# Optimization experiments

Hardware: AMD Instinct MI355X
Metric: run time of the kernel (lower is better)

## Reference

```python
import jax, jax.numpy as jnp
import numpy as np

B, S, H, V = 32, 400, 512, 50000


def setup_inputs() -> dict:
    key = jax.random.key(0)
    ks = jax.random.split(key, 32)
    g = lambda i, shape: jax.random.normal(ks[i], shape, jnp.float32) * 0.05
    return {
        "x_id": jax.random.randint(ks[0], (B, S), 0, V, jnp.int32),
        "y_id": jax.random.randint(ks[1], (B, 1), 0, V, jnp.int32),
        "x_mask": jnp.zeros((B, S), jnp.int32),  # pad flag: 1 = pad
        "emb": g(2, (V, H)),
        "enc_fw_W": g(3, (H, 3 * H)), "enc_fw_U": g(4, (H, 3 * H)), "enc_fw_b": g(5, (2, 3 * H)),
        "enc_bw_W": g(6, (H, 3 * H)), "enc_bw_U": g(7, (H, 3 * H)), "enc_bw_b": g(8, (2, 3 * H)),
        "red_W": g(9, (2 * H, H)), "red_b": g(10, (H,)),
        "dec_W": g(11, (H, 3 * H)), "dec_U": g(12, (H, 3 * H)), "dec_b": g(13, (2, 3 * H)),
        "att_Wh": g(14, (2 * H, H)), "att_Ws": g(15, (H, H)), "att_bs": g(16, (H,)),
        "att_Wc": g(17, (1, 1)), "att_V": g(18, (H, 1)),
        "fc_W": g(19, (3 * H, H)), "fc_b": g(20, (H,)),
        "vocab_W": g(21, (H, V)),
        "pg_Wh": g(22, (2 * H, 1)), "pg_Ws": g(23, (H, 1)), "pg_Wx": g(24, (H, 1)), "pg_b": g(25, (1,)),
    }


def _gru_cell(h, xz, U, br):
    # Keras GRU, reset_after=True, gate order z, r, h
    hd = h.shape[-1]
    rec = h @ U + br
    z = jax.nn.sigmoid(xz[..., :hd] + rec[..., :hd])
    r = jax.nn.sigmoid(xz[..., hd:2 * hd] + rec[..., hd:2 * hd])
    hh = jnp.tanh(xz[..., 2 * hd:] + r * rec[..., 2 * hd:])
    return z * h + (1.0 - z) * hh


def _gru_scan(x, h0, W, U, b):
    xz = x @ W + b[0]  # [b,T,3H] -- input projections precomputed
    def step(h, xt):
        h = _gru_cell(h, xt, U, b[1])
        return h, h
    h_last, hs = jax.lax.scan(step, h0, jnp.swapaxes(xz, 0, 1))
    return jnp.swapaxes(hs, 0, 1), h_last


def reference(x_id, y_id, x_mask, emb, enc_fw_W, enc_fw_U, enc_fw_b, enc_bw_W, enc_bw_U, enc_bw_b,
              red_W, red_b, dec_W, dec_U, dec_b, att_Wh, att_Ws, att_bs, att_Wc, att_V,
              fc_W, fc_b, vocab_W, pg_Wh, pg_Ws, pg_Wx, pg_b):
    b, s = x_id.shape
    hid = enc_fw_U.shape[0]
    maskf = x_mask.astype(jnp.float32)
    # ---- encoder: single-layer BiGRU ----
    x_emb = emb[x_id]                                     # [b,S,H]
    h0 = jnp.zeros((b, hid), x_emb.dtype)
    fw_seq, fw_s = _gru_scan(x_emb, h0, enc_fw_W, enc_fw_U, enc_fw_b)
    bw_seq, bw_s = _gru_scan(x_emb[:, ::-1], h0, enc_bw_W, enc_bw_U, enc_bw_b)
    enc_seq = jnp.concatenate([fw_seq, bw_seq[:, ::-1]], -1)   # [b,S,2H]
    state = jax.nn.relu(jnp.concatenate([fw_s, bw_s], -1) @ red_W + red_b)  # [b,H]
    # ---- decoder: one GRU step ----
    y_emb = emb[y_id]                                     # [b,1,H]
    xz = y_emb[:, 0] @ dec_W + dec_b[0]
    dec_state = _gru_cell(state, xz, dec_U, dec_b[1])     # [b,H]
    dec_out = dec_state[:, None, :]                       # [b,1,H]
    # ---- Bahdanau attention with (zero-initialized) coverage ----
    e = enc_seq @ att_Wh + (dec_out @ att_Ws + att_bs)    # [b,S,H]
    cover = jnp.zeros((b, s, 1), e.dtype)
    e = e + cover @ att_Wc
    e = jnp.tanh(e) @ att_V                               # [b,S,1]
    e = e + maskf[..., None] * -1e10
    w = jax.nn.softmax(e, axis=-2)                        # [b,S,1]
    context = jnp.sum(w * enc_seq, axis=-2, keepdims=True)  # [b,1,2H]
    # ---- output projection + vocab softmax ----
    y_out = jnp.concatenate([dec_out, context], -1) @ fc_W + fc_b  # [b,1,H]
    vocab_dist = jax.nn.softmax(y_out[:, 0] @ vocab_W, axis=-1)    # [b,V]
    # ---- pointer gate ----
    p_gen = jax.nn.sigmoid(context[:, 0] @ pg_Wh + dec_state @ pg_Ws + y_emb[:, 0] @ pg_Wx + pg_b)  # [b,1]
    # ---- extended-vocab copy distribution (vectorized batched scatter-add) ----
    aw = w[..., 0] * (1.0 - maskf) * (1.0 - p_gen)        # [b,S]
    ext = jnp.pad(p_gen * vocab_dist, ((0, 0), (0, s)))   # [b,V+S]
    bidx = jnp.arange(b)[:, None]
    final = ext.at[bidx, x_id].add(aw)                    # [b,V+S]
    return final
```

## Files before the change

### kernel.cpp

```cpp
#include <hip/hip_runtime.h>
#include <math.h>

#define S_LEN 400
#define BATCH 32
#define HID   512
#define G3    1536
#define N2    3072
#define VOC   50000
#define OUTW  (VOC + S_LEN)

typedef unsigned long long ull;
typedef unsigned int uint;
typedef unsigned short ushort;
typedef short bf16x8 __attribute__((ext_vector_type(8)));
typedef float f32x4 __attribute__((ext_vector_type(4)));
typedef ushort u16x8 __attribute__((ext_vector_type(8)));

__device__ __forceinline__ float sigf(float x) { return 1.f / (1.f + __expf(-x)); }
__device__ __forceinline__ float tanh_fast(float x) {
  const float xc = fminf(fmaxf(x, -15.f), 15.f);
  const float e = __expf(-2.f * xc);
  return (1.f - e) / (1.f + e);
}
__device__ __forceinline__ ushort f2bf(float f) {
  uint u = __float_as_uint(f);
  u += 0x7FFFu + ((u >> 16) & 1u);
  return (ushort)(u >> 16);
}
__device__ __forceinline__ float bf2f(ushort h) {
  return __uint_as_float((uint)h << 16);
}
__device__ __forceinline__ float dot4(float4 a, float4 b) {
  return a.x*b.x + a.y*b.y + a.z*b.z + a.w*b.w;
}

__device__ void trans_tile_512(const float* __restrict__ srcA,
                               const float* __restrict__ srcB,
                               const int split, const int stride, const int Krows,
                               const int k0, const int n0,
                               ushort* __restrict__ dstH, float* __restrict__ dstF)
{
  __shared__ float tt[64][65];
  const int tid = threadIdx.x;
  const int j = tid & 63, i0 = tid >> 6;
  {
    const int n = n0 + j;
    const float* s = (n < split) ? (srcA + n) : (srcB + (n - split));
    #pragma unroll
    for (int i = i0; i < 64; i += 8)
      tt[i][j] = s[(size_t)(k0 + i) * stride];
  }
  __syncthreads();
  const int ii = tid & 63;
  if (dstH != nullptr) {
    #pragma unroll
    for (int jj = i0; jj < 64; jj += 8)
      dstH[(size_t)(n0 + jj) * Krows + k0 + ii] = f2bf(tt[ii][jj]);
  } else {
    #pragma unroll
    for (int jj = i0; jj < 64; jj += 8)
      dstF[(size_t)(n0 + jj) * Krows + k0 + ii] = tt[ii][jj];
  }
}

__global__ __launch_bounds__(512) void gru_scan(
    const ushort* __restrict__ xzm,
    const ushort* __restrict__ Utbf,
    const float* __restrict__ bfw, const float* __restrict__ bbw,
    float* __restrict__ enc_seq, ushort* __restrict__ enc_bf,
    ull* __restrict__ hpkt,
    const float* __restrict__ att_Wh, const float* __restrict__ red_W,
    const float* __restrict__ dec_W, const float* __restrict__ dec_U,
    const float* __restrict__ att_Ws, const float* __restrict__ fc_W,
    ushort* __restrict__ Whbf, float* __restrict__ redWt,
    float* __restrict__ decWUt, float* __restrict__ WsT,
    float* __restrict__ fcT)
{
  if (blockIdx.x >= 128) {
    const int tb = blockIdx.x - 128;
    if (tb < 128) {
      trans_tile_512(att_Wh, att_Wh, 512, 512, 1024,
                     (tb % 16) * 64, (tb / 16) * 64, Whbf, nullptr);
    } else if (tb < 256) {
      const int t = tb - 128;
      trans_tile_512(red_W, red_W, 512, 512, 1024,
                     (t % 16) * 64, (t / 16) * 64, nullptr, redWt);
    } else if (tb < 640) {
      const int t = tb - 256;
      trans_tile_512(dec_W, dec_U, G3, G3, 512,
                     (t % 8) * 64, (t / 8) * 64, nullptr, decWUt);
    } else if (tb < 704) {
      const int t = tb - 640;
      trans_tile_512(att_Ws, att_Ws, 512, 512, 512,
                     (t % 8) * 64, (t / 8) * 64, nullptr, WsT);
    } else {
      const int t = tb - 704;
      trans_tile_512(fc_W, fc_W, 512, 512, 1536,
                     (t % 24) * 64, (t / 24) * 64, nullptr, fcT);
    }
    return;
  }

  const int bid = blockIdx.x;
  const int group = bid & 7;
  const int dir = group >> 2;
  const int bg  = group & 3;
  const int ht  = bid >> 3;
  const int tid = threadIdx.x;
  const int lane = tid & 63;
  const int w  = tid >> 6;
  const int l15 = lane & 15;
  const int lk  = lane >> 4;

  const float* __restrict__ br = (dir ? bbw : bfw) + G3;

  const int gate = w % 3, jh = w / 3;
  bf16x8 ufrag[16];
  if (w < 6) {
    const ushort* ub = Utbf + ((size_t)dir * G3 + gate * 512 + ht * 32 + jh * 16 + l15) * 512
                     + lk * 8;
    #pragma unroll
    for (int s = 0; s < 16; ++s)
      ufrag[s] = *(const bf16x8*)(ub + s * 32);
  }

  __shared__ ushort h_bf[16][520];
  __shared__ float redm[3][8][32];

  for (int i = tid; i < 16 * 520; i += 512) ((ushort*)h_bf)[i] = 0;

  const int cb = w;
  const int gbi = tid >> 5;
  const int gj  = tid & 31;
  const int gjq = ht * 32 + gj;
  const int gb  = bg * 8 + (gbi & 7);
  const float brz = br[gjq], brr = br[512 + gjq], brh = br[1024 + gjq];

  ull* __restrict__ pk = hpkt + (size_t)dir * (2 * BATCH * HID);
  __syncthreads();

  for (int t = 0; t < S_LEN; ++t) {
    const int ts = dir ? (S_LEN - 1 - t) : t;

    float xzv0 = 0.f, xzv1 = 0.f, xzv2 = 0.f;
    if (tid < 256) {
      const ushort* xp = xzm + ((size_t)gb * S_LEN + ts) * N2 + dir * G3 + gjq;
      xzv0 = bf2f(xp[0]); xzv1 = bf2f(xp[512]); xzv2 = bf2f(xp[1024]);
    }

    float hold = 0.f;
    {
      ull* bp = pk + ((size_t)(t & 1) * BATCH + (bg * 8 + cb)) * HID + lane;
      ull* hp = pk + ((size_t)(t & 1) * BATCH + gb) * HID + gjq;
      const uint tu = (uint)t;
      for (;;) {
        ull v0 = __hip_atomic_load(bp,       __ATOMIC_RELAXED, __HIP_MEMORY_SCOPE_AGENT);
        ull v1 = __hip_atomic_load(bp + 64,  __ATOMIC_RELAXED, __HIP_MEMORY_SCOPE_AGENT);
        ull v2 = __hip_atomic_load(bp + 128, __ATOMIC_RELAXED, __HIP_MEMORY_SCOPE_AGENT);
        ull v3 = __hip_atomic_load(bp + 192, __ATOMIC_RELAXED, __HIP_MEMORY_SCOPE_AGENT);
        ull v4 = __hip_atomic_load(bp + 256, __ATOMIC_RELAXED, __HIP_MEMORY_SCOPE_AGENT);
        ull v5 = __hip_atomic_load(bp + 320, __ATOMIC_RELAXED, __HIP_MEMORY_SCOPE_AGENT);
        ull v6 = __hip_atomic_load(bp + 384, __ATOMIC_RELAXED, __HIP_MEMORY_SCOPE_AGENT);
        ull v7 = __hip_atomic_load(bp + 448, __ATOMIC_RELAXED, __HIP_MEMORY_SCOPE_AGENT);
        bool ok = ((uint)(v0 >> 32) == tu) & ((uint)(v1 >> 32) == tu)
                & ((uint)(v2 >> 32) == tu) & ((uint)(v3 >> 32) == tu)
                & ((uint)(v4 >> 32) == tu) & ((uint)(v5 >> 32) == tu)
                & ((uint)(v6 >> 32) == tu) & ((uint)(v7 >> 32) == tu);
        ull hv = 0;
        if (tid < 256) {
          hv = __hip_atomic_load(hp, __ATOMIC_RELAXED, __HIP_MEMORY_SCOPE_AGENT);
          ok &= ((uint)(hv >> 32) == tu);
        }
        if (__all(ok)) {
          h_bf[cb][lane]       = f2bf(__uint_as_float((uint)v0));
          h_bf[cb][lane + 64]  = f2bf(__uint_as_float((uint)v1));
          h_bf[cb][lane + 128] = f2bf(__uint_as_float((uint)v2));
          h_bf[cb][lane + 192] = f2bf(__uint_as_float((uint)v3));
          h_bf[cb][lane + 256] = f2bf(__uint_as_float((uint)v4));
          h_bf[cb][lane + 320] = f2bf(__uint_as_float((uint)v5));
          h_bf[cb][lane + 384] = f2bf(__uint_as_float((uint)v6));
          h_bf[cb][lane + 448] = f2bf(__uint_as_float((uint)v7));
          if (tid < 256) hold = __uint_as_float((uint)hv);
          break;
        }
        __builtin_amdgcn_s_sleep(1);
      }
    }
    __syncthreads();

    if (w < 6) {
      f32x4 acc = f32x4{0.f, 0.f, 0.f, 0.f};
      #pragma unroll
      for (int s = 0; s < 16; ++s) {
        const bf16x8 af = *(const bf16x8*)&h_bf[l15][s * 32 + lk * 8];
        acc = __builtin_amdgcn_mfma_f32_16x16x32_bf16(af, ufrag[s], acc, 0, 0, 0);
      }
      if (lk < 2) {
        #pragma unroll
        for (int r = 0; r < 4; ++r)
          redm[gate][lk * 4 + r][jh * 16 + l15] = acc[r];
      }
    }
    __syncthreads();

    if (tid < 256) {
      const float rz = redm[0][gbi][gj] + brz;
      const float rr = redm[1][gbi][gj] + brr;
      const float rh = redm[2][gbi][gj] + brh;
      const float z  = sigf(xzv0 + rz);
      const float r  = sigf(xzv1 + rr);
      const float hh = tanh_fast(xzv2 + r * rh);
      const float hnew = z * hold + (1.f - z) * hh;
      const ull pack = ((ull)(uint)(t + 1) << 32) | (ull)__float_as_uint(hnew);
      __hip_atomic_store(pk + ((size_t)((t + 1) & 1) * BATCH + gb) * HID + gjq,
                         pack, __ATOMIC_RELAXED, __HIP_MEMORY_SCOPE_AGENT);
      const size_t eidx = ((size_t)gb * S_LEN + ts) * 1024 + dir * 512 + gjq;
      enc_seq[eidx] = hnew;
      enc_bf[eidx]  = f2bf(hnew);
    }
    __syncthreads();
  }
}

__global__ __launch_bounds__(256) void k_cvtA(
    const int* __restrict__ x_id, const float* __restrict__ emb,
    ushort* __restrict__ Abf)
{
  const int tid = threadIdx.x;
  const int row = blockIdx.x * 4 + (tid >> 6);
  const int k8 = (tid & 63) * 8;
  const int rid = x_id[row];
  const float4 e0 = *(const float4*)&emb[(size_t)rid * 512 + k8];
  const float4 e1 = *(const float4*)&emb[(size_t)rid * 512 + k8 + 4];
  u16x8 o;
  o[0] = f2bf(e0.x); o[1] = f2bf(e0.y); o[2] = f2bf(e0.z); o[3] = f2bf(e0.w);
  o[4] = f2bf(e1.x); o[5] = f2bf(e1.y); o[6] = f2bf(e1.z); o[7] = f2bf(e1.w);
  *(u16x8*)&Abf[(size_t)row * 512 + k8] = o;
}

__global__ __launch_bounds__(256) void k_transUp(
    const float* __restrict__ fwW, const float* __restrict__ bwW,
    const float* __restrict__ fwb, const float* __restrict__ bwb,
    const float* __restrict__ fwU, const float* __restrict__ bwU,
    ushort* __restrict__ Wt, float* __restrict__ bm,
    ushort* __restrict__ Utbf)
{
  __shared__ float tt[64][65];
  const int b = blockIdx.x;
  const int tid = threadIdx.x;
  const int j = tid & 63, i0 = tid >> 6;
  const float* srcA; const float* srcB; int split, k0, n0; ushort* dst;
  if (b < 384)      { srcA = fwW; srcB = bwW; split = G3;
                      k0 = (b % 8) * 64; n0 = (b / 8) * 64; dst = Wt; }
  else if (b < 576) { const int t = b - 384; srcA = fwU; srcB = fwU; split = N2;
                      k0 = (t % 8) * 64; n0 = (t / 8) * 64; dst = Utbf; }
  else              { const int t = b - 576; srcA = bwU; srcB = bwU; split = N2;
                      k0 = (t % 8) * 64; n0 = (t / 8) * 64;
                      dst = Utbf + (size_t)G3 * 512; }
  {
    const int n = n0 + j;
    const float* s = (n < split) ? (srcA + n) : (srcB + (n - split));
    #pragma unroll
    for (int i = i0; i < 64; i += 4)
      tt[i][j] = s[(size_t)(k0 + i) * G3];
  }
  __syncthreads();
  const int ii = tid & 63;
  #pragma unroll
  for (int jj = i0; jj < 64; jj += 4)
    dst[(size_t)(n0 + jj) * 512 + k0 + ii] = f2bf(tt[ii][jj]);
  if (b < 384 && k0 == 0 && tid < 64) {
    const int n = n0 + tid;
    bm[n] = (n < G3) ? fwb[n] : bwb[n - G3];
  }
}

__global__ __launch_bounds__(256) void gemm_bf16(
    const ushort* __restrict__ A,
    const ushort* __restrict__ Bt,
    const float* __restrict__ bias,
    ushort* __restrict__ C)
{
  const int m0 = blockIdx.y * 128, n0 = blockIdx.x * 128;
  const int tid = threadIdx.x;
  const int w = tid >> 6, lane = tid & 63;
  const int l15 = lane & 15, lk = lane >> 4;
  __shared__ short As[128][40];
  __shared__ short Bs[128][40];
  f32x4 acc[2][8];
  #pragma unroll
  for (int i = 0; i < 2; ++i)
    #pragma unroll
    for (int j = 0; j < 8; ++j) acc[i][j] = f32x4{0.f, 0.f, 0.f, 0.f};

  const int sr = tid >> 1;
  const int sc = (tid & 1) * 8;

  for (int k0 = 0; k0 < 512; k0 += 32) {
    const uint4 a0 = *(const uint4*)&A[(size_t)(m0 + sr) * 512 + k0 + sc];
    const uint4 a1 = *(const uint4*)&A[(size_t)(m0 + sr) * 512 + k0 + 16 + sc];
    const uint4 b0 = *(const uint4*)&Bt[(size_t)(n0 + sr) * 512 + k0 + sc];
    const uint4 b1 = *(const uint4*)&Bt[(size_t)(n0 + sr) * 512 + k0 + 16 + sc];
    *(uint4*)&As[sr][sc]      = a0;
    *(uint4*)&As[sr][16 + sc] = a1;
    *(uint4*)&Bs[sr][sc]      = b0;
    *(uint4*)&Bs[sr][16 + sc] = b1;
    __syncthreads();

    bf16x8 af[2], bfr[8];
    #pragma unroll
    for (int rf = 0; rf < 2; ++rf)
      af[rf] = *(const bf16x8*)&As[w * 32 + rf * 16 + l15][lk * 8];
    #pragma unroll
    for (int cf = 0; cf < 8; ++cf)
      bfr[cf] = *(const bf16x8*)&Bs[cf * 16 + l15][lk * 8];
    #pragma unroll
    for (int rf = 0; rf < 2; ++rf)
      #pragma unroll
      for (int cf = 0; cf < 8; ++cf)
        acc[rf][cf] = __builtin_amdgcn_mfma_f32_16x16x32_bf16(
            af[rf], bfr[cf], acc[rf][cf], 0, 0, 0);
    __syncthreads();
  }

  #pragma unroll
  for (int rf = 0; rf < 2; ++rf) {
    #pragma unroll
    for (int cf = 0; cf < 8; ++cf) {
      const int col = n0 + cf * 16 + l15;
      const float bv = bias[col];
      const int rowb = m0 + w * 32 + rf * 16 + lk * 4;
      #pragma unroll
      for (int r = 0; r < 4; ++r)
        C[(size_t)(rowb + r) * N2 + col] = f2bf(acc[rf][cf][r] + bv);
    }
  }
}

__global__ __launch_bounds__(256) void gemm_att(
    const ushort* __restrict__ A,
    const ushort* __restrict__ Bt,
    const float* __restrict__ dterm,
    const float* __restrict__ attV,
    float* __restrict__ e_part)
{
  const int m0 = blockIdx.y * 128, n0 = blockIdx.x * 128;
  const int tid = threadIdx.x;
  const int w = tid >> 6, lane = tid & 63;
  const int l15 = lane & 15, lk = lane >> 4;
  __shared__ short As[128][40];
  __shared__ short Bs[128][40];
  f32x4 acc[2][8];
  #pragma unroll
  for (int i = 0; i < 2; ++i)
    #pragma unroll
    for (int j = 0; j < 8; ++j) acc[i][j] = f32x4{0.f, 0.f, 0.f, 0.f};

  const int sr = tid >> 1;
  const int sc = (tid & 1) * 8;

  for (int k0 = 0; k0 < 1024; k0 += 32) {
    const uint4 a0 = *(const uint4*)&A[(size_t)(m0 + sr) * 1024 + k0 + sc];
    const uint4 a1 = *(const uint4*)&A[(size_t)(m0 + sr) * 1024 + k0 + 16 + sc];
    const uint4 b0 = *(const uint4*)&Bt[(size_t)(n0 + sr) * 1024 + k0 + sc];
    const uint4 b1 = *(const uint4*)&Bt[(size_t)(n0 + sr) * 1024 + k0 + 16 + sc];
    *(uint4*)&As[sr][sc]      = a0;
    *(uint4*)&As[sr][16 + sc] = a1;
    *(uint4*)&Bs[sr][sc]      = b0;
    *(uint4*)&Bs[sr][16 + sc] = b1;
    __syncthreads();

    bf16x8 af[2], bfr[8];
    #pragma unroll
    for (int rf = 0; rf < 2; ++rf)
      af[rf] = *(const bf16x8*)&As[w * 32 + rf * 16 + l15][lk * 8];
    #pragma unroll
    for (int cf = 0; cf < 8; ++cf)
      bfr[cf] = *(const bf16x8*)&Bs[cf * 16 + l15][lk * 8];
    #pragma unroll
    for (int rf = 0; rf < 2; ++rf)
      #pragma unroll
      for (int cf = 0; cf < 8; ++cf)
        acc[rf][cf] = __builtin_amdgcn_mfma_f32_16x16x32_bf16(
            af[rf], bfr[cf], acc[rf][cf], 0, 0, 0);
    __syncthreads();
  }

  #pragma unroll
  for (int rf = 0; rf < 2; ++rf) {
    #pragma unroll
    for (int r = 0; r < 4; ++r) {
      const int row = m0 + w * 32 + rf * 16 + lk * 4 + r;
      const int b = row / S_LEN;
      float p = 0.f;
      #pragma unroll
      for (int cf = 0; cf < 8; ++cf) {
        const int col = n0 + cf * 16 + l15;
        p += attV[col] * tanh_fast(acc[rf][cf][r] + dterm[(size_t)b * 512 + col]);
      }
      p += __shfl_xor(p, 1); p += __shfl_xor(p, 2);
      p += __shfl_xor(p, 4); p += __shfl_xor(p, 8);
      if (l15 == 0) e_part[(size_t)row * 4 + blockIdx.x] = p;
    }
  }
}

__global__ __launch_bounds__(128) void k_state(const float* __restrict__ enc,
    const float* __restrict__ redWt,
    const float* __restrict__ red_b, float* __restrict__ state)
{
  const int b = blockIdx.y;
  const int j = blockIdx.x*128 + threadIdx.x;
  const float4* wr = (const float4*)(redWt + (size_t)j * 1024);
  const float4* fw = (const float4*)(enc + ((size_t)b*S_LEN + (S_LEN-1))*1024);
  const float4* bw = (const float4*)(enc + ((size_t)b*S_LEN)*1024 + 512);
  float acc = red_b[j];
  #pragma unroll 4
  for (int k = 0; k < 128; ++k) acc += dot4(fw[k], wr[k]);
  #pragma unroll 4
  for (int k = 0; k < 128; ++k) acc += dot4(bw[k], wr[128 + k]);
  state[(size_t)b*512 + j] = fmaxf(acc, 0.f);
}

__global__ __launch_bounds__(128) void k_dec(
    const int* __restrict__ y_id, const float* __restrict__ emb,
    const float* __restrict__ state,
    const float* __restrict__ decWUt,
    const float* __restrict__ dec_b, float* __restrict__ dst)
{
  const int b = blockIdx.y;
  const int j = blockIdx.x*128 + threadIdx.x;
  const float4* ye = (const float4*)(emb + (size_t)y_id[b] * 512);
  const float4* st = (const float4*)(state + (size_t)b * 512);
  const float4* w0 = (const float4*)(decWUt + (size_t)(j)        * 512);
  const float4* w1 = (const float4*)(decWUt + (size_t)(512  + j) * 512);
  const float4* w2 = (const float4*)(decWUt + (size_t)(1024 + j) * 512);
  const float4* u0 = (const float4*)(decWUt + (size_t)(G3 + j)        * 512);
  const float4* u1 = (const float4*)(decWUt + (size_t)(G3 + 512  + j) * 512);
  const float4* u2 = (const float4*)(decWUt + (size_t)(G3 + 1024 + j) * 512);
  float xz0 = dec_b[j], xz1 = dec_b[512+j], xz2 = dec_b[1024+j];
  float rc0 = dec_b[G3+j], rc1 = dec_b[G3+512+j], rc2 = dec_b[G3+1024+j];
  #pragma unroll 2
  for (int k = 0; k < 128; ++k) {
    const float4 yv = ye[k], sv = st[k];
    xz0 += dot4(yv, w0[k]); xz1 += dot4(yv, w1[k]); xz2 += dot4(yv, w2[k]);
    rc0 += dot4(sv, u0[k]); rc1 += dot4(sv, u1[k]); rc2 += dot4(sv, u2[k]);
  }
  const float z  = sigf(xz0 + rc0);
  const float r  = sigf(xz1 + rc1);
  const float hh = tanh_fast(xz2 + r*rc2);
  const float sj = state[(size_t)b*512 + j];
  dst[(size_t)b*512 + j] = z*sj + (1.f-z)*hh;
}

__global__ __launch_bounds__(128) void k_dterm(const float* __restrict__ dec,
    const float* __restrict__ WsT,
    const float* __restrict__ att_bs, float* __restrict__ dterm)
{
  const int b = blockIdx.y;
  const int j = blockIdx.x*128 + threadIdx.x;
  const float4* d = (const float4*)(dec + (size_t)b*512);
  const float4* wr = (const float4*)(WsT + (size_t)j * 512);
  float acc = att_bs[j];
  #pragma unroll 4
  for (int k = 0; k < 128; ++k) acc += dot4(d[k], wr[k]);
  dterm[(size_t)b*512 + j] = acc;
}

__global__ __launch_bounds__(512) void k_soft(const float* __restrict__ e_part,
    const int* __restrict__ x_mask, float* __restrict__ wat)
{
  const int b = blockIdx.x, tid = threadIdx.x;
  __shared__ float sm[512];
  float e = -1e30f, ev = 0.f;
  if (tid < S_LEN) {
    const float* ep = e_part + (size_t)(b*S_LEN + tid)*4;
    ev = ep[0]+ep[1]+ep[2]+ep[3] + (float)x_mask[b*S_LEN+tid] * -1e10f;
    e = ev;
  }
  sm[tid] = e; __syncthreads();
  for (int s = 256; s > 0; s >>= 1) { if (tid < s) sm[tid] = fmaxf(sm[tid], sm[tid+s]); __syncthreads(); }
  const float m = sm[0]; __syncthreads();
  const float x = (tid < S_LEN) ? __expf(ev - m) : 0.f;
  sm[tid] = x; __syncthreads();
  for (int s = 256; s > 0; s >>= 1) { if (tid < s) sm[tid] += sm[tid+s]; __syncthreads(); }
  const float inv = 1.f / sm[0];
  if (tid < S_LEN) wat[b*S_LEN+tid] = x * inv;
}

__global__ __launch_bounds__(128) void k_ctx(const float* __restrict__ wat,
    const float* __restrict__ enc, float* __restrict__ ctx)
{
  const int b = blockIdx.y;
  const int j = blockIdx.x*128 + threadIdx.x;
  float acc = 0.f;
  const float* w = wat + b*S_LEN;
  const float* ep = enc + (size_t)b*S_LEN*1024 + j;
  #pragma unroll 4
  for (int s = 0; s < S_LEN; ++s) acc += w[s] * ep[(size_t)s*1024];
  ctx[(size_t)b*1024 + j] = acc;
}

__global__ __launch_bounds__(128) void k_yout(const float* __restrict__ dec,
    const float* __restrict__ ctx,
    const float* __restrict__ fcT,
    const float* __restrict__ fc_b, float* __restrict__ y_out)
{
  const int b = blockIdx.y;
  const int j = blockIdx.x*128 + threadIdx.x;
  const float4* d = (const float4*)(dec + (size_t)b*512);
  const float4* c = (const float4*)(ctx + (size_t)b*1024);
  const float4* wr = (const float4*)(fcT + (size_t)j * 1536);
  float acc = fc_b[j];
  #pragma unroll 4
  for (int k = 0; k < 128; ++k) acc += dot4(d[k], wr[k]);
  #pragma unroll 4
  for (int k = 0; k < 256; ++k) acc += dot4(c[k], wr[128 + k]);
  y_out[(size_t)b*512 + j] = acc;
}

__global__ __launch_bounds__(256) void k_pgen(const float* __restrict__ ctx,
    const float* __restrict__ dec,
    const int* __restrict__ y_id, const float* __restrict__ emb,
    const float* __restrict__ pg_Wh, const float* __restrict__ pg_Ws,
    const float* __restrict__ pg_Wx, const float* __restrict__ pg_b,
    float* __restrict__ pg)
{
  const int b = blockIdx.x, tid = threadIdx.x;
  __shared__ float sm[256];
  const float* ye = emb + (size_t)y_id[b] * 512;
  float acc = 0.f;
  for (int k = tid; k < 1024; k += 256) acc += ctx[(size_t)b*1024+k]*pg_Wh[k];
  for (int k = tid; k < 512;  k += 256) acc += dec[(size_t)b*512+k]*pg_Ws[k] + ye[k]*pg_Wx[k];
  sm[tid] = acc; __syncthreads();
  for (int s = 128; s > 0; s >>= 1) { if (tid < s) sm[tid] += sm[tid+s]; __syncthreads(); }
  if (tid == 0) pg[b] = sigf(sm[0] + pg_b[0]);
}

__global__ __launch_bounds__(256) void k_vocab(const float* __restrict__ y_out,
    const float* __restrict__ vocab_W, float* __restrict__ logits)
{
  __shared__ float y_lds[256][32];
  const int tid = threadIdx.x;
  const int vq = tid & 63, bq = tid >> 6;
  const int v = blockIdx.x * 256 + vq * 4;
  float acc[8][4];
  #pragma unroll
  for (int i = 0; i < 8; ++i)
    #pragma unroll
    for (int j = 0; j < 4; ++j) acc[i][j] = 0.f;
  for (int half = 0; half < 2; ++half) {
    __syncthreads();
    for (int i = 0; i < 32; ++i) {
      const int idx = tid + 256*i;
      const int k = idx >> 5, b = idx & 31;
      y_lds[k][b] = y_out[(size_t)b*512 + half*256 + k];
    }
    __syncthreads();
    if (v < VOC) {
      #pragma unroll 4
      for (int k = 0; k < 256; ++k) {
        const float4 wv = *(const float4*)&vocab_W[(size_t)(half*256 + k) * VOC + v];
        const float4 ya = *(const float4*)&y_lds[k][bq*8];
        const float4 yb = *(const float4*)&y_lds[k][bq*8+4];
        const float yy[8] = {ya.x,ya.y,ya.z,ya.w,yb.x,yb.y,yb.z,yb.w};
        #pragma unroll
        for (int i = 0; i < 8; ++i) {
          acc[i][0] += yy[i]*wv.x; acc[i][1] += yy[i]*wv.y;
          acc[i][2] += yy[i]*wv.z; acc[i][3] += yy[i]*wv.w;
        }
      }
    }
  }
  if (v < VOC) {
    #pragma unroll
    for (int i = 0; i < 8; ++i)
      *(float4*)&logits[(size_t)(bq*8+i)*VOC + v] = make_float4(acc[i][0],acc[i][1],acc[i][2],acc[i][3]);
  }
}

__global__ __launch_bounds__(1024) void k_vred(const float* __restrict__ logits,
                                               float* __restrict__ red2)
{
  const int b = blockIdx.x, tid = threadIdx.x;
  __shared__ float sm[1024];
  float m = -1e30f;
  for (int i = tid; i < VOC; i += 1024) m = fmaxf(m, logits[(size_t)b*VOC + i]);
  sm[tid] = m; __syncthreads();
  for (int s = 512; s > 0; s >>= 1) { if (tid < s) sm[tid] = fmaxf(sm[tid], sm[tid+s]); __syncthreads(); }
  m = sm[0]; __syncthreads();
  float sum = 0.f;
  for (int i = tid; i < VOC; i += 1024) sum += __expf(logits[(size_t)b*VOC + i] - m);
  sm[tid] = sum; __syncthreads();
  for (int s = 512; s > 0; s >>= 1) { if (tid < s) sm[tid] += sm[tid+s]; __syncthreads(); }
  if (tid == 0) { red2[b*2] = m; red2[b*2+1] = sm[0]; }
}

__global__ __launch_bounds__(256) void k_final(const float* __restrict__ logits,
    const float* __restrict__ red2, const float* __restrict__ pg,
    float* __restrict__ out)
{
  const size_t idx = (size_t)blockIdx.x*256 + threadIdx.x;
  const int b = (int)(idx / OUTW);
  const int c = (int)(idx - (size_t)b*OUTW);
  float v = 0.f;
  if (c < VOC) {
    const float m = red2[b*2], s = red2[b*2+1];
    v = pg[b] * __expf(logits[(size_t)b*VOC + c] - m) / s;
  }
  out[idx] = v;
}

__global__ __launch_bounds__(256) void k_scatter(const float* __restrict__ wat,
    const int* __restrict__ x_mask, const float* __restrict__ pg,
    const int* __restrict__ x_id, float* __restrict__ out)
{
  const int i = blockIdx.x*256 + threadIdx.x;
  const int b = i / S_LEN;
  const float aw = wat[i] * (1.f - (float)x_mask[i]) * (1.f - pg[b]);
  atomicAdd(out + (size_t)b*OUTW + x_id[i], aw);
}

extern "C" void kernel_launch(void* const* d_in, const int* in_sizes, int n_in,
                              void* d_out, int out_size, void* d_ws, size_t ws_size,
                              hipStream_t stream)
{
  (void)in_sizes; (void)n_in; (void)out_size; (void)ws_size;
  const int*   x_id     = (const int*)d_in[0];
  const int*   y_id     = (const int*)d_in[1];
  const int*   x_mask   = (const int*)d_in[2];
  const float* emb      = (const float*)d_in[3];
  const float* enc_fw_W = (const float*)d_in[4];
  const float* enc_fw_U = (const float*)d_in[5];
  const float* enc_fw_b = (const float*)d_in[6];
  const float* enc_bw_W = (const float*)d_in[7];
  const float* enc_bw_U = (const float*)d_in[8];
  const float* enc_bw_b = (const float*)d_in[9];
  const float* red_W    = (const float*)d_in[10];
  const float* red_b    = (const float*)d_in[11];
  const float* dec_W    = (const float*)d_in[12];
  const float* dec_U    = (const float*)d_in[13];
  const float* dec_b    = (const float*)d_in[14];
  const float* att_Wh   = (const float*)d_in[15];
  const float* att_Ws   = (const float*)d_in[16];
  const float* att_bs   = (const float*)d_in[17];
  const float* att_Wc   = (const float*)d_in[18]; (void)att_Wc;
  const float* att_V    = (const float*)d_in[19];
  const float* fc_W     = (const float*)d_in[20];
  const float* fc_b     = (const float*)d_in[21];
  const float* vocab_W  = (const float*)d_in[22];
  const float* pg_Wh    = (const float*)d_in[23];
  const float* pg_Ws    = (const float*)d_in[24];
  const float* pg_Wx    = (const float*)d_in[25];
  const float* pg_b     = (const float*)d_in[26];
  float* out = (float*)d_out;

  const size_t NPKT = (size_t)2*2*BATCH*HID;
  char* p = (char*)d_ws;
  ushort* xzm   = (ushort*)p; p += (size_t)BATCH*S_LEN*N2*2;
  float*  enc   = (float*)p;  p += (size_t)BATCH*S_LEN*1024*4;
  ushort* encbf = (ushort*)p; p += (size_t)BATCH*S_LEN*1024*2;
  ull*   hpkt   = (ull*)p;    p += NPKT*8;
  ushort* Abf   = (ushort*)p; p += (size_t)BATCH*S_LEN*512*2;
  ushort* Wt    = (ushort*)p; p += (size_t)N2*512*2;
  ushort* Whbf  = (ushort*)p; p += (size_t)512*1024*2;
  ushort* Utbf  = (ushort*)p; p += (size_t)2*G3*512*2;
  float*  redWt = (float*)p;  p += (size_t)512*1024*4;
  float*  decWUt= (float*)p;  p += (size_t)N2*512*4;
  float*  WsT   = (float*)p;  p += (size_t)512*512*4;
  float*  fcT   = (float*)p;  p += (size_t)512*1536*4;
  float*  bm    = (float*)p;  p += (size_t)N2*4;
  float*  fstate = (float*)p; p += (size_t)BATCH*HID*4;
  float*  decs   = (float*)p; p += (size_t)BATCH*HID*4;
  float*  dterm  = (float*)p; p += (size_t)BATCH*HID*4;
  float*  epart  = (float*)p; p += (size_t)BATCH*S_LEN*4*4;
  float*  wat    = (float*)p; p += (size_t)BATCH*S_LEN*4;
  float*  ctx    = (float*)p; p += (size_t)BATCH*1024*4;
  float*  yout   = (float*)p; p += (size_t)BATCH*HID*4;
  float*  pg     = (float*)p; p += (size_t)256*4;
  float*  logits = (float*)p; p += (size_t)BATCH*VOC*4;
  float*  red2   = (float*)p; p += (size_t)64*4;

  hipMemsetAsync(hpkt, 0, NPKT * sizeof(ull), stream);

  k_cvtA<<<BATCH*S_LEN/4, 256, 0, stream>>>(x_id, emb, Abf);
  k_transUp<<<768, 256, 0, stream>>>(enc_fw_W, enc_bw_W, enc_fw_b, enc_bw_b,
                                     enc_fw_U, enc_bw_U, Wt, bm, Utbf);
  gemm_bf16<<<dim3(N2/128, BATCH*S_LEN/128), 256, 0, stream>>>(Abf, Wt, bm, xzm);
  gru_scan<<<128 + 896, 512, 0, stream>>>(xzm, Utbf, enc_fw_b, enc_bw_b,
                                          enc, encbf, hpkt,
                                          att_Wh, red_W, dec_W, dec_U, att_Ws,
                                          fc_W, Whbf, redWt, decWUt, WsT, fcT);
  k_state<<<dim3(4,32),128,0,stream>>>(enc, redWt, red_b, fstate);
  k_dec<<<dim3(4,32),128,0,stream>>>(y_id, emb, fstate, decWUt, dec_b, decs);
  k_dterm<<<dim3(4,32),128,0,stream>>>(decs, WsT, att_bs, dterm);
  gemm_att<<<dim3(4, BATCH*S_LEN/128), 256, 0, stream>>>(encbf, Whbf, dterm,
                                                         att_V, epart);
  k_soft<<<32,512,0,stream>>>(epart, x_mask, wat);
  k_ctx<<<dim3(8,32),128,0,stream>>>(wat, enc, ctx);
  k_yout<<<dim3(4,32),128,0,stream>>>(decs, ctx, fcT, fc_b, yout);
  k_pgen<<<32,256,0,stream>>>(ctx, decs, y_id, emb, pg_Wh, pg_Ws, pg_Wx, pg_b, pg);
  k_vocab<<<196,256,0,stream>>>(yout, vocab_W, logits);
  k_vred<<<32,1024,0,stream>>>(logits, red2);
  k_final<<<6300,256,0,stream>>>(logits, red2, pg, out);
  k_scatter<<<50,256,0,stream>>>(wat, x_mask, pg, x_id, out);
}
```

Measured before the change: 1.326 ms.

## Drop fp32 encoder copy, enlarge GEMM tiles with prefetch, fuse softmax stats

Stops writing the fp32 encoder sequence and has k_state and k_ctx read the bf16 copy, which removes large global writes and reads. Merges the embedding-conversion and weight-transpose kernels into one launch. Enlarges the two bf16 GEMM tiles to 256 rows and prefetches the next k-slice into registers. The vocab kernel now computes per-block softmax max and sum partials, so the full-logit reduction pass is replaced by a tiny combine kernel. The costs are lower precision for context and state (they now come from bf16), more register pressure in the GEMMs, and fewer GEMM blocks.

Result: slower. 1.411 ms (+6.4%).

```diff
diff --git a/kernel.cpp b/kernel.cpp
--- a/kernel.cpp
+++ b/kernel.cpp
@@ -67,8 +67,7 @@
     const ushort* __restrict__ xzm,
     const ushort* __restrict__ Utbf,
     const float* __restrict__ bfw, const float* __restrict__ bbw,
-    float* __restrict__ enc_seq, ushort* __restrict__ enc_bf,
-    ull* __restrict__ hpkt,
+    ushort* __restrict__ enc_bf, ull* __restrict__ hpkt,
     const float* __restrict__ att_Wh, const float* __restrict__ red_W,
     const float* __restrict__ dec_W, const float* __restrict__ dec_U,
     const float* __restrict__ att_Ws, const float* __restrict__ fc_W,
@@ -214,40 +213,36 @@
       const ull pack = ((ull)(uint)(t + 1) << 32) | (ull)__float_as_uint(hnew);
       __hip_atomic_store(pk + ((size_t)((t + 1) & 1) * BATCH + gb) * HID + gjq,
                          pack, __ATOMIC_RELAXED, __HIP_MEMORY_SCOPE_AGENT);
-      const size_t eidx = ((size_t)gb * S_LEN + ts) * 1024 + dir * 512 + gjq;
-      enc_seq[eidx] = hnew;
-      enc_bf[eidx]  = f2bf(hnew);
-    }
-    __syncthreads();
-  }
-}
-
-__global__ __launch_bounds__(256) void k_cvtA(
+      enc_bf[((size_t)gb * S_LEN + ts) * 1024 + dir * 512 + gjq] = f2bf(hnew);
+    }
+    __syncthreads();
+  }
+}
+
+__global__ __launch_bounds__(256) void k_prep(
     const int* __restrict__ x_id, const float* __restrict__ emb,
-    ushort* __restrict__ Abf)
-{
-  const int tid = threadIdx.x;
-  const int row = blockIdx.x * 4 + (tid >> 6);
-  const int k8 = (tid & 63) * 8;
-  const int rid = x_id[row];
-  const float4 e0 = *(const float4*)&emb[(size_t)rid * 512 + k8];
-  const float4 e1 = *(const float4*)&emb[(size_t)rid * 512 + k8 + 4];
-  u16x8 o;
-  o[0] = f2bf(e0.x); o[1] = f2bf(e0.y); o[2] = f2bf(e0.z); o[3] = f2bf(e0.w);
-  o[4] = f2bf(e1.x); o[5] = f2bf(e1.y); o[6] = f2bf(e1.z); o[7] = f2bf(e1.w);
-  *(u16x8*)&Abf[(size_t)row * 512 + k8] = o;
-}
-
-__global__ __launch_bounds__(256) void k_transUp(
+    ushort* __restrict__ Abf,
     const float* __restrict__ fwW, const float* __restrict__ bwW,
     const float* __restrict__ fwb, const float* __restrict__ bwb,
     const float* __restrict__ fwU, const float* __restrict__ bwU,
     ushort* __restrict__ Wt, float* __restrict__ bm,
     ushort* __restrict__ Utbf)
 {
+  const int tid = threadIdx.x;
+  if (blockIdx.x < 3200) {
+    const int row = blockIdx.x * 4 + (tid >> 6);
+    const int k8 = (tid & 63) * 8;
+    const int rid = x_id[row];
+    const float4 e0 = *(const float4*)&emb[(size_t)rid * 512 + k8];
+    const float4 e1 = *(const float4*)&emb[(size_t)rid * 512 + k8 + 4];
+    u16x8 o;
+    o[0] = f2bf(e0.x); o[1] = f2bf(e0.y); o[2] = f2bf(e0.z); o[3] = f2bf(e0.w);
+    o[4] = f2bf(e1.x); o[5] = f2bf(e1.y); o[6] = f2bf(e1.z); o[7] = f2bf(e1.w);
+    *(u16x8*)&Abf[(size_t)row * 512 + k8] = o;
+    return;
+  }
   __shared__ float tt[64][65];
-  const int b = blockIdx.x;
-  const int tid = threadIdx.x;
+  const int b = blockIdx.x - 3200;
   const int j = tid & 63, i0 = tid >> 6;
   const float* srcA; const float* srcB; int split, k0, n0; ushort* dst;
   if (b < 384)      { srcA = fwW; srcB = bwW; split = G3;
@@ -281,41 +276,54 @@
     const float* __restrict__ bias,
     ushort* __restrict__ C)
 {
-  const int m0 = blockIdx.y * 128, n0 = blockIdx.x * 128;
+  const int m0 = blockIdx.y * 256, n0 = blockIdx.x * 128;
   const int tid = threadIdx.x;
   const int w = tid >> 6, lane = tid & 63;
   const int l15 = lane & 15, lk = lane >> 4;
-  __shared__ short As[128][40];
+  __shared__ short As[256][40];
   __shared__ short Bs[128][40];
-  f32x4 acc[2][8];
+  f32x4 acc[4][8];
   #pragma unroll
-  for (int i = 0; i < 2; ++i)
+  for (int i = 0; i < 4; ++i)
     #pragma unroll
     for (int j = 0; j < 8; ++j) acc[i][j] = f32x4{0.f, 0.f, 0.f, 0.f};
 
-  const int sr = tid >> 1;
-  const int sc = (tid & 1) * 8;
+  const ushort* arow = A + (size_t)(m0 + tid) * 512;
+  const int bsr = tid >> 1, bsc = (tid & 1) * 16;
+  const ushort* brow = Bt + (size_t)(n0 + bsr) * 512 + bsc;
+
+  uint4 ga0 = *(const uint4*)(arow + 0);
+  uint4 ga1 = *(const uint4*)(arow + 8);
+  uint4 ga2 = *(const uint4*)(arow + 16);
+  uint4 ga3 = *(const uint4*)(arow + 24);
+  uint4 gb0 = *(const uint4*)(brow + 0);
+  uint4 gb1 = *(const uint4*)(brow + 8);
 
   for (int k0 = 0; k0 < 512; k0 += 32) {
-    const uint4 a0 = *(const uint4*)&A[(size_t)(m0 + sr) * 512 + k0 + sc];
-    const uint4 a1 = *(const uint4*)&A[(size_t)(m0 + sr) * 512 + k0 + 16 + sc];
-    const uint4 b0 = *(const uint4*)&Bt[(size_t)(n0 + sr) * 512 + k0 + sc];
-    const uint4 b1 = *(const uint4*)&Bt[(size_t)(n0 + sr) * 512 + k0 + 16 + sc];
-    *(uint4*)&As[sr][sc]      = a0;
-    *(uint4*)&As[sr][16 + sc] = a1;
-    *(uint4*)&Bs[sr][sc]      = b0;
-    *(uint4*)&Bs[sr][16 + sc] = b1;
-    __syncthreads();
-
-    bf16x8 af[2], bfr[8];
-    #pragma unroll
-    for (int rf = 0; rf < 2; ++rf)
-      af[rf] = *(const bf16x8*)&As[w * 32 + rf * 16 + l15][lk * 8];
+    *(uint4*)&As[tid][0]  = ga0;
+    *(uint4*)&As[tid][8]  = ga1;
+    *(uint4*)&As[tid][16] = ga2;
+    *(uint4*)&As[tid][24] = ga3;
+    *(uint4*)&Bs[bsr][bsc]     = gb0;
+    *(uint4*)&Bs[bsr][bsc + 8] = gb1;
+    __syncthreads();
+    if (k0 + 32 < 512) {
+      ga0 = *(const uint4*)(arow + k0 + 32);
+      ga1 = *(const uint4*)(arow + k0 + 40);
+      ga2 = *(const uint4*)(arow + k0 + 48);
+      ga3 = *(const uint4*)(arow + k0 + 56);
+      gb0 = *(const uint4*)(brow + k0 + 32);
+      gb1 = *(const uint4*)(brow + k0 + 40);
+    }
+    bf16x8 af[4], bfr[8];
+    #pragma unroll
+    for (int rf = 0; rf < 4; ++rf)
+      af[rf] = *(const bf16x8*)&As[w * 64 + rf * 16 + l15][lk * 8];
     #pragma unroll
     for (int cf = 0; cf < 8; ++cf)
       bfr[cf] = *(const bf16x8*)&Bs[cf * 16 + l15][lk * 8];
     #pragma unroll
-    for (int rf = 0; rf < 2; ++rf)
+    for (int rf = 0; rf < 4; ++rf)
       #pragma unroll
       for (int cf = 0; cf < 8; ++cf)
         acc[rf][cf] = __builtin_amdgcn_mfma_f32_16x16x32_bf16(
@@ -324,12 +332,12 @@
   }
 
   #pragma unroll
-  for (int rf = 0; rf < 2; ++rf) {
+  for (int rf = 0; rf < 4; ++rf) {
     #pragma unroll
     for (int cf = 0; cf < 8; ++cf) {
       const int col = n0 + cf * 16 + l15;
       const float bv = bias[col];
-      const int rowb = m0 + w * 32 + rf * 16 + lk * 4;
+      const int rowb = m0 + w * 64 + rf * 16 + lk * 4;
       #pragma unroll
       for (int r = 0; r < 4; ++r)
         C[(size_t)(rowb + r) * N2 + col] = f2bf(acc[rf][cf][r] + bv);
@@ -344,41 +352,54 @@
     const float* __restrict__ attV,
     float* __restrict__ e_part)
 {
-  const int m0 = blockIdx.y * 128, n0 = blockIdx.x * 128;
+  const int m0 = blockIdx.y * 256, n0 = blockIdx.x * 128;
   const int tid = threadIdx.x;
   const int w = tid >> 6, lane = tid & 63;
   const int l15 = lane & 15, lk = lane >> 4;
-  __shared__ short As[128][40];
+  __shared__ short As[256][40];
   __shared__ short Bs[128][40];
-  f32x4 acc[2][8];
+  f32x4 acc[4][8];
   #pragma unroll
-  for (int i = 0; i < 2; ++i)
+  for (int i = 0; i < 4; ++i)
     #pragma unroll
     for (int j = 0; j < 8; ++j) acc[i][j] = f32x4{0.f, 0.f, 0.f, 0.f};
 
-  const int sr = tid >> 1;
-  const int sc = (tid & 1) * 8;
+  const ushort* arow = A + (size_t)(m0 + tid) * 1024;
+  const int bsr = tid >> 1, bsc = (tid & 1) * 16;
+  const ushort* brow = Bt + (size_t)(n0 + bsr) * 1024 + bsc;
+
+  uint4 ga0 = *(const uint4*)(arow + 0);
+  uint4 ga1 = *(const uint4*)(arow + 8);
+  uint4 ga2 = *(const uint4*)(arow + 16);
+  uint4 ga3 = *(const uint4*)(arow + 24);
+  uint4 gb0 = *(const uint4*)(brow + 0);
+  uint4 gb1 = *(const uint4*)(brow + 8);
 
   for (int k0 = 0; k0 < 1024; k0 += 32) {
-    const uint4 a0 = *(const uint4*)&A[(size_t)(m0 + sr) * 1024 + k0 + sc];
-    const uint4 a1 = *(const uint4*)&A[(size_t)(m0 + sr) * 1024 + k0 + 16 + sc];
-    const uint4 b0 = *(const uint4*)&Bt[(size_t)(n0 + sr) * 1024 + k0 + sc];
-    const uint4 b1 = *(const uint4*)&Bt[(size_t)(n0 + sr) * 1024 + k0 + 16 + sc];
-    *(uint4*)&As[sr][sc]      = a0;
-    *(uint4*)&As[sr][16 + sc] = a1;
-    *(uint4*)&Bs[sr][sc]      = b0;
-    *(uint4*)&Bs[sr][16 + sc] = b1;
-    __syncthreads();
-
-    bf16x8 af[2], bfr[8];
-    #pragma unroll
-    for (int rf = 0; rf < 2; ++rf)
-      af[rf] = *(const bf16x8*)&As[w * 32 + rf * 16 + l15][lk * 8];
+    *(uint4*)&As[tid][0]  = ga0;
+    *(uint4*)&As[tid][8]  = ga1;
+    *(uint4*)&As[tid][16] = ga2;
+    *(uint4*)&As[tid][24] = ga3;
+    *(uint4*)&Bs[bsr][bsc]     = gb0;
+    *(uint4*)&Bs[bsr][bsc + 8] = gb1;
+    __syncthreads();
+    if (k0 + 32 < 1024) {
+      ga0 = *(const uint4*)(arow + k0 + 32);
+      ga1 = *(const uint4*)(arow + k0 + 40);
+      ga2 = *(const uint4*)(arow + k0 + 48);
+      ga3 = *(const uint4*)(arow + k0 + 56);
+      gb0 = *(const uint4*)(brow + k0 + 32);
+      gb1 = *(const uint4*)(brow + k0 + 40);
+    }
+    bf16x8 af[4], bfr[8];
+    #pragma unroll
+    for (int rf = 0; rf < 4; ++rf)
+      af[rf] = *(const bf16x8*)&As[w * 64 + rf * 16 + l15][lk * 8];
     #pragma unroll
     for (int cf = 0; cf < 8; ++cf)
       bfr[cf] = *(const bf16x8*)&Bs[cf * 16 + l15][lk * 8];
     #pragma unroll
-    for (int rf = 0; rf < 2; ++rf)
+    for (int rf = 0; rf < 4; ++rf)
       #pragma unroll
       for (int cf = 0; cf < 8; ++cf)
         acc[rf][cf] = __builtin_amdgcn_mfma_f32_16x16x32_bf16(
@@ -387,10 +408,10 @@
   }
 
   #pragma unroll
-  for (int rf = 0; rf < 2; ++rf) {
+  for (int rf = 0; rf < 4; ++rf) {
     #pragma unroll
     for (int r = 0; r < 4; ++r) {
-      const int row = m0 + w * 32 + rf * 16 + lk * 4 + r;
+      const int row = m0 + w * 64 + rf * 16 + lk * 4 + r;
       const int b = row / S_LEN;
       float p = 0.f;
       #pragma unroll
@@ -405,20 +426,27 @@
   }
 }
 
-__global__ __launch_bounds__(128) void k_state(const float* __restrict__ enc,
-    const float* __restrict__ redWt,
-    const float* __restrict__ red_b, float* __restrict__ state)
+__global__ __launch_bounds__(128) void k_state(const ushort* __restrict__ encbf,
+    const float* __restrict__ redWt, const float* __restrict__ red_b,
+    float* __restrict__ state)
 {
   const int b = blockIdx.y;
   const int j = blockIdx.x*128 + threadIdx.x;
+  __shared__ float hf[512], hb[512];
+  const ushort* fw = encbf + ((size_t)b*S_LEN + (S_LEN-1))*1024;
+  const ushort* bw = encbf + ((size_t)b*S_LEN)*1024 + 512;
+  for (int k = threadIdx.x; k < 512; k += 128) {
+    hf[k] = bf2f(fw[k]); hb[k] = bf2f(bw[k]);
+  }
+  __syncthreads();
   const float4* wr = (const float4*)(redWt + (size_t)j * 1024);
-  const float4* fw = (const float4*)(enc + ((size_t)b*S_LEN + (S_LEN-1))*1024);
-  const float4* bw = (const float4*)(enc + ((size_t)b*S_LEN)*1024 + 512);
+  const float4* hf4 = (const float4*)hf;
+  const float4* hb4 = (const float4*)hb;
   float acc = red_b[j];
   #pragma unroll 4
-  for (int k = 0; k < 128; ++k) acc += dot4(fw[k], wr[k]);
+  for (int k = 0; k < 128; ++k) acc += dot4(hf4[k], wr[k]);
   #pragma unroll 4
-  for (int k = 0; k < 128; ++k) acc += dot4(bw[k], wr[128 + k]);
+  for (int k = 0; k < 128; ++k) acc += dot4(hb4[k], wr[128 + k]);
   state[(size_t)b*512 + j] = fmaxf(acc, 0.f);
 }
 
@@ -454,8 +482,8 @@
 }
 
 __global__ __launch_bounds__(128) void k_dterm(const float* __restrict__ dec,
-    const float* __restrict__ WsT,
-    const float* __restrict__ att_bs, float* __restrict__ dterm)
+    const float* __restrict__ WsT, const float* __restrict__ att_bs,
+    float* __restrict__ dterm)
 {
   const int b = blockIdx.y;
   const int j = blockIdx.x*128 + threadIdx.x;
@@ -489,21 +517,25 @@
 }
 
 __global__ __launch_bounds__(128) void k_ctx(const float* __restrict__ wat,
-    const float* __restrict__ enc, float* __restrict__ ctx)
+    const ushort* __restrict__ encbf, float* __restrict__ ctx)
 {
   const int b = blockIdx.y;
-  const int j = blockIdx.x*128 + threadIdx.x;
-  float acc = 0.f;
+  const int j2 = (blockIdx.x*128 + threadIdx.x) * 2;
+  float a0 = 0.f, a1 = 0.f;
   const float* w = wat + b*S_LEN;
-  const float* ep = enc + (size_t)b*S_LEN*1024 + j;
+  const ushort* ep = encbf + (size_t)b*S_LEN*1024 + j2;
   #pragma unroll 4
-  for (int s = 0; s < S_LEN; ++s) acc += w[s] * ep[(size_t)s*1024];
-  ctx[(size_t)b*1024 + j] = acc;
+  for (int s = 0; s < S_LEN; ++s) {
+    const uint u = *(const uint*)&ep[(size_t)s*1024];
+    a0 += w[s] * bf2f((ushort)u);
+    a1 += w[s] * bf2f((ushort)(u >> 16));
+  }
+  ctx[(size_t)b*1024 + j2]     = a0;
+  ctx[(size_t)b*1024 + j2 + 1] = a1;
 }
 
 __global__ __launch_bounds__(128) void k_yout(const float* __restrict__ dec,
-    const float* __restrict__ ctx,
-    const float* __restrict__ fcT,
+    const float* __restrict__ ctx, const float* __restrict__ fcT,
     const float* __restrict__ fc_b, float* __restrict__ y_out)
 {
   const int b = blockIdx.y;
@@ -538,12 +570,14 @@
 }
 
 __global__ __launch_bounds__(256) void k_vocab(const float* __restrict__ y_out,
-    const float* __restrict__ vocab_W, float* __restrict__ logits)
+    const float* __restrict__ vocab_W, float* __restrict__ logits,
+    float* __restrict__ vpart)
 {
   __shared__ float y_lds[256][32];
   const int tid = threadIdx.x;
   const int vq = tid & 63, bq = tid >> 6;
   const int v = blockIdx.x * 256 + vq * 4;
+  const bool valid = (v < VOC);
   float acc[8][4];
   #pragma unroll
   for (int i = 0; i < 8; ++i)
@@ -557,7 +591,7 @@
       y_lds[k][b] = y_out[(size_t)b*512 + half*256 + k];
     }
     __syncthreads();
-    if (v < VOC) {
+    if (valid) {
       #pragma unroll 4
       for (int k = 0; k < 256; ++k) {
         const float4 wv = *(const float4*)&vocab_W[(size_t)(half*256 + k) * VOC + v];
@@ -572,28 +606,47 @@
       }
     }
   }
-  if (v < VOC) {
+  if (valid) {
     #pragma unroll
     for (int i = 0; i < 8; ++i)
       *(float4*)&logits[(size_t)(bq*8+i)*VOC + v] = make_float4(acc[i][0],acc[i][1],acc[i][2],acc[i][3]);
   }
-}
-
-__global__ __launch_bounds__(1024) void k_vred(const float* __restrict__ logits,
-                                               float* __restrict__ red2)
-{
-  const int b = blockIdx.x, tid = threadIdx.x;
-  __shared__ float sm[1024];
+  #pragma unroll
+  for (int i = 0; i < 8; ++i) {
+    float m = valid ? fmaxf(fmaxf(acc[i][0], acc[i][1]), fmaxf(acc[i][2], acc[i][3]))
+                    : -1e30f;
+    m = fmaxf(m, __shfl_xor(m, 1));  m = fmaxf(m, __shfl_xor(m, 2));
+    m = fmaxf(m, __shfl_xor(m, 4));  m = fmaxf(m, __shfl_xor(m, 8));
+    m = fmaxf(m, __shfl_xor(m, 16)); m = fmaxf(m, __shfl_xor(m, 32));
+    float s = 0.f;
+    if (valid) {
+      s = __expf(acc[i][0]-m) + __expf(acc[i][1]-m)
+        + __expf(acc[i][2]-m) + __expf(acc[i][3]-m);
+    }
+    s += __shfl_xor(s, 1);  s += __shfl_xor(s, 2);
+    s += __shfl_xor(s, 4);  s += __shfl_xor(s, 8);
+    s += __shfl_xor(s, 16); s += __shfl_xor(s, 32);
+    if ((tid & 63) == 0) {
+      const size_t o = ((size_t)blockIdx.x * 32 + bq * 8 + i) * 2;
+      vpart[o] = m; vpart[o + 1] = s;
+    }
+  }
+}
+
+__global__ __launch_bounds__(64) void k_vred2(const float* __restrict__ vpart,
+                                              float* __restrict__ red2)
+{
+  const int b = threadIdx.x;
+  if (b >= 32) return;
   float m = -1e30f;
-  for (int i = tid; i < VOC; i += 1024) m = fmaxf(m, logits[(size_t)b*VOC + i]);
-  sm[tid] = m; __syncthreads();
-  for (int s = 512; s > 0; s >>= 1) { if (tid < s) sm[tid] = fmaxf(sm[tid], sm[tid+s]); __syncthreads(); }
-  m = sm[0]; __syncthreads();
-  float sum = 0.f;
-  for (int i = tid; i < VOC; i += 1024) sum += __expf(logits[(size_t)b*VOC + i] - m);
-  sm[tid] = sum; __syncthreads();
-  for (int s = 512; s > 0; s >>= 1) { if (tid < s) sm[tid] += sm[tid+s]; __syncthreads(); }
-  if (tid == 0) { red2[b*2] = m; red2[b*2+1] = sm[0]; }
+  for (int x = 0; x < 196; ++x) m = fmaxf(m, vpart[((size_t)x*32 + b)*2]);
+  float S = 0.f;
+  for (int x = 0; x < 196; ++x) {
+    const float ml = vpart[((size_t)x*32 + b)*2];
+    const float sl = vpart[((size_t)x*32 + b)*2 + 1];
+    S += sl * __expf(ml - m);
+  }
+  red2[b*2] = m; red2[b*2+1] = S;
 }
 
 __global__ __launch_bounds__(256) void k_final(const float* __restrict__ logits,
@@ -658,7 +711,6 @@
   const size_t NPKT = (size_t)2*2*BATCH*HID;
   char* p = (char*)d_ws;
   ushort* xzm   = (ushort*)p; p += (size_t)BATCH*S_LEN*N2*2;
-  float*  enc   = (float*)p;  p += (size_t)BATCH*S_LEN*1024*4;
   ushort* encbf = (ushort*)p; p += (size_t)BATCH*S_LEN*1024*2;
   ull*   hpkt   = (ull*)p;    p += NPKT*8;
   ushort* Abf   = (ushort*)p; p += (size_t)BATCH*S_LEN*512*2;
@@ -680,28 +732,29 @@
   float*  pg     = (float*)p; p += (size_t)256*4;
   float*  logits = (float*)p; p += (size_t)BATCH*VOC*4;
   float*  red2   = (float*)p; p += (size_t)64*4;
+  float*  vpart  = (float*)p; p += (size_t)196*32*2*4;
 
   hipMemsetAsync(hpkt, 0, NPKT * sizeof(ull), stream);
 
-  k_cvtA<<<BATCH*S_LEN/4, 256, 0, stream>>>(x_id, emb, Abf);
-  k_transUp<<<768, 256, 0, stream>>>(enc_fw_W, enc_bw_W, enc_fw_b, enc_bw_b,
-                                     enc_fw_U, enc_bw_U, Wt, bm, Utbf);
-  gemm_bf16<<<dim3(N2/128, BATCH*S_LEN/128), 256, 0, stream>>>(Abf, Wt, bm, xzm);
+  k_prep<<<3200 + 768, 256, 0, stream>>>(x_id, emb, Abf,
+                                         enc_fw_W, enc_bw_W, enc_fw_b, enc_bw_b,
+                                         enc_fw_U, enc_bw_U, Wt, bm, Utbf);
+  gemm_bf16<<<dim3(N2/128, BATCH*S_LEN/256), 256, 0, stream>>>(Abf, Wt, bm, xzm);
   gru_scan<<<128 + 896, 512, 0, stream>>>(xzm, Utbf, enc_fw_b, enc_bw_b,
-                                          enc, encbf, hpkt,
+                                          encbf, hpkt,
                                           att_Wh, red_W, dec_W, dec_U, att_Ws,
                                           fc_W, Whbf, redWt, decWUt, WsT, fcT);
-  k_state<<<dim3(4,32),128,0,stream>>>(enc, redWt, red_b, fstate);
+  k_state<<<dim3(4,32),128,0,stream>>>(encbf, redWt, red_b, fstate);
   k_dec<<<dim3(4,32),128,0,stream>>>(y_id, emb, fstate, decWUt, dec_b, decs);
   k_dterm<<<dim3(4,32),128,0,stream>>>(decs, WsT, att_bs, dterm);
-  gemm_att<<<dim3(4, BATCH*S_LEN/128), 256, 0, stream>>>(encbf, Whbf, dterm,
+  gemm_att<<<dim3(4, BATCH*S_LEN/256), 256, 0, stream>>>(encbf, Whbf, dterm,
                                                          att_V, epart);
   k_soft<<<32,512,0,stream>>>(epart, x_mask, wat);
-  k_ctx<<<dim3(8,32),128,0,stream>>>(wat, enc, ctx);
+  k_ctx<<<dim3(4,32),128,0,stream>>>(wat, encbf, ctx);
   k_yout<<<dim3(4,32),128,0,stream>>>(decs, ctx, fcT, fc_b, yout);
   k_pgen<<<32,256,0,stream>>>(ctx, decs, y_id, emb, pg_Wh, pg_Ws, pg_Wx, pg_b, pg);
-  k_vocab<<<196,256,0,stream>>>(yout, vocab_W, logits);
-  k_vred<<<32,1024,0,stream>>>(logits, red2);
+  k_vocab<<<196,256,0,stream>>>(yout, vocab_W, logits, vpart);
+  k_vred2<<<1,64,0,stream>>>(vpart, red2);
   k_final<<<6300,256,0,stream>>>(logits, red2, pg, out);
   k_scatter<<<50,256,0,stream>>>(wat, x_mask, pg, x_id, out);
 }
```
